# Kernel optimization log

Hardware: AMD Instinct MI355X
Metric: run time of the kernel (lower is better)

## Reference

```python
import jax, jax.numpy as jnp
import numpy as np

N = 100000   # num nodes
E = 640000   # num edges
IN, H, OUT = 6, 128, 1
BN_EPS = 1e-5


def setup_inputs() -> dict:
    key = jax.random.key(0)
    ks = jax.random.split(key, 12)
    x = jax.random.normal(ks[0], (N, IN), dtype=jnp.float32)
    edge_index = jax.random.randint(ks[1], (2, E), 0, N, dtype=jnp.int64)
    def lin(k, fin, fout):
        s = 1.0 / np.sqrt(fin)
        return jax.random.uniform(k, (fin, fout), jnp.float32, -s, s)
    return {
        "x": x,
        "edge_index": edge_index,
        "W1": lin(ks[2], IN, H),  "b1": jnp.zeros((H,), jnp.float32),
        "W2": lin(ks[3], H, H),   "b2": jnp.zeros((H,), jnp.float32),
        "W3": lin(ks[4], H, OUT), "b3": jnp.zeros((OUT,), jnp.float32),
        "g1": jnp.ones((H,), jnp.float32),  "be1": jnp.zeros((H,), jnp.float32),
        "g2": jnp.ones((H,), jnp.float32),  "be2": jnp.zeros((H,), jnp.float32),
    }


def _gcn_norm(edge_index):
    # add self-loops, then symmetric normalization D^-1/2 (A+I) D^-1/2
    loop = jnp.arange(N, dtype=edge_index.dtype)
    src = jnp.concatenate([edge_index[0], loop])
    dst = jnp.concatenate([edge_index[1], loop])
    deg = jax.ops.segment_sum(jnp.ones_like(dst, dtype=jnp.float32), dst, num_segments=N)
    dis = jnp.where(deg > 0, jax.lax.rsqrt(deg), 0.0)
    norm = dis[src] * dis[dst]  # (E+N,)
    return src, dst, norm


def _conv(h, W, b, src, dst, norm):
    m = h @ W                                   # (N, out) linear transform first
    msg = m[src] * norm[:, None]                # gather + edge scaling
    return jax.ops.segment_sum(msg, dst, num_segments=N) + b


def _bn(h, g, be):
    mu = h.mean(axis=0)
    var = h.var(axis=0)  # biased, as torch BN uses for normalization
    return g * (h - mu) * jax.lax.rsqrt(var + BN_EPS) + be


def reference(x, edge_index, W1, b1, W2, b2, W3, b3, g1, be1, g2, be2):
    src, dst, norm = _gcn_norm(edge_index)
    h = jax.nn.relu(_bn(_conv(x, W1, b1, src, dst, norm), g1, be1))
    h = jax.nn.relu(_bn(_conv(h, W2, b2, src, dst, norm), g2, be2))
    out = _conv(h, W3, b3, src, dst, norm)
    return jax.nn.sigmoid(out)  # (N, 1) risk scores
```

## Files before the change

### kernel.cpp

```cpp
#include <hip/hip_runtime.h>
#include <hip/hip_bf16.h>
#include <math.h>

#define HDIM 128
#define BN_EPS 1e-5f
#define CHUNK 512
#define TM 64
#define LDA 132

__device__ __forceinline__ int eget(const void* ei, long long pos, int is64) {
    return is64 ? (int)((const long long*)ei)[pos] : ((const int*)ei)[pos];
}
__device__ __forceinline__ unsigned short f2bf(float f) {
    unsigned int u = __float_as_uint(f);
    u += 0x7fffu + ((u >> 16) & 1u);
    return (unsigned short)(u >> 16);
}
__device__ __forceinline__ unsigned int pack2bf(float lo, float hi) {
    return (unsigned int)f2bf(lo) | ((unsigned int)f2bf(hi) << 16);
}
__device__ __forceinline__ float bflo(unsigned int u) {
    return __uint_as_float(u << 16);
}
__device__ __forceinline__ float bfhi(unsigned int u) {
    return __uint_as_float(u & 0xffff0000u);
}

__global__ void k_detect(const int* ei32, int* flag) {
    if (threadIdx.x == 0) {
        int nz = 0;
        for (int k = 0; k < 64; ++k) nz += (ei32[2 * k + 1] != 0);
        *flag = (nz < 8) ? 1 : 0;
    }
}

__global__ void k_count(const void* ei, const int* flag, int* cnt, int E) {
    int e = blockIdx.x * blockDim.x + threadIdx.x;
    if (e < E) {
        int d = eget(ei, (long long)E + e, *flag);
        atomicAdd(&cnt[d], 1);
    }
}

__global__ void k_dis(const int* cnt, float* dis, int N) {
    int i = blockIdx.x * blockDim.x + threadIdx.x;
    if (i < N) dis[i] = rsqrtf((float)(cnt[i] + 1));
}

__global__ void k_scan1(const int* cnt, int* bsum, int N) {
    __shared__ int s[256];
    int t = threadIdx.x;
    int i = blockIdx.x * CHUNK + t;
    int v = 0;
    if (i < N) v += cnt[i];
    if (i + 256 < N && t + 256 < CHUNK) v += cnt[i + 256];
    s[t] = v; __syncthreads();
    for (int o = 128; o > 0; o >>= 1) {
        if (t < o) s[t] += s[t + o];
        __syncthreads();
    }
    if (t == 0) bsum[blockIdx.x] = s[0];
}

__global__ void k_scan2(int* bsum, int nb) {
    __shared__ int s[512];
    int t = threadIdx.x;
    int carry = 0;
    for (int base = 0; base < nb; base += 512) {
        int i = base + t;
        int v = (i < nb) ? bsum[i] : 0;
        s[t] = v; __syncthreads();
        for (int o = 1; o < 512; o <<= 1) {
            int add = (t >= o) ? s[t - o] : 0;
            __syncthreads();
            s[t] += add;
            __syncthreads();
        }
        if (i < nb) bsum[i] = carry + s[t] - v;
        carry += s[511];
        __syncthreads();
    }
}

__global__ void k_scan3(const int* cnt, const int* bsum, int* rowptr, int N) {
    __shared__ int s[CHUNK];
    int t = threadIdx.x;
    int i = blockIdx.x * CHUNK + t;
    int v = (i < N) ? cnt[i] : 0;
    s[t] = v; __syncthreads();
    for (int o = 1; o < CHUNK; o <<= 1) {
        int add = (t >= o) ? s[t - o] : 0;
        __syncthreads();
        s[t] += add;
        __syncthreads();
    }
    if (i < N) rowptr[i] = bsum[blockIdx.x] + s[t] - v;
    if (i == N - 1) rowptr[N] = bsum[blockIdx.x] + s[t];
}

__global__ void k_fillcsr(const void* ei, const int* flag, const float* dis,
                          const int* rowptr, int* fill, int* esrc, float* enorm, int E) {
    int e = blockIdx.x * blockDim.x + threadIdx.x;
    if (e < E) {
        int is64 = *flag;
        int s = eget(ei, e, is64);
        int d = eget(ei, (long long)E + e, is64);
        int pos = rowptr[d] + atomicAdd(&fill[d], 1);
        esrc[pos] = s;
        enorm[pos] = dis[s] * dis[d];
    }
}

__global__ void k_padx(const float* __restrict__ x, float* __restrict__ xp, int N) {
    int t = blockIdx.x * blockDim.x + threadIdx.x;
    if (t < N * 8) {
        int i = t >> 3, c = t & 7;
        xp[t] = (c < 6) ? x[i * 6 + c] : 0.f;
    }
}

__global__ void k_gath_x(const float* __restrict__ xp, const int* __restrict__ rowptr,
                         const int* __restrict__ esrc, const float* __restrict__ enorm,
                         const float* __restrict__ dis, float* __restrict__ aggx, int N) {
    int i = blockIdx.x * blockDim.x + threadIdx.x;
    if (i >= N) return;
    float d = dis[i], d2 = d * d;
    float4 A = *(const float4*)&xp[i * 8];
    float2 B = *(const float2*)&xp[i * 8 + 4];
    float a0 = A.x * d2, a1 = A.y * d2, a2 = A.z * d2;
    float a3 = A.w * d2, a4 = B.x * d2, a5 = B.y * d2;
    int p = rowptr[i], pe = rowptr[i + 1];
    for (; p + 4 <= pe; p += 4) {
        int s0 = esrc[p], s1 = esrc[p + 1], s2 = esrc[p + 2], s3 = esrc[p + 3];
        float n0 = enorm[p], n1 = enorm[p + 1], n2 = enorm[p + 2], n3 = enorm[p + 3];
        float4 A0 = *(const float4*)&xp[s0 * 8];
        float2 B0 = *(const float2*)&xp[s0 * 8 + 4];
        float4 A1 = *(const float4*)&xp[s1 * 8];
        float2 B1 = *(const float2*)&xp[s1 * 8 + 4];
        float4 A2 = *(const float4*)&xp[s2 * 8];
        float2 B2 = *(const float2*)&xp[s2 * 8 + 4];
        float4 A3 = *(const float4*)&xp[s3 * 8];
        float2 B3 = *(const float2*)&xp[s3 * 8 + 4];
        a0 += (A0.x * n0 + A1.x * n1) + (A2.x * n2 + A3.x * n3);
        a1 += (A0.y * n0 + A1.y * n1) + (A2.y * n2 + A3.y * n3);
        a2 += (A0.z * n0 + A1.z * n1) + (A2.z * n2 + A3.z * n3);
        a3 += (A0.w * n0 + A1.w * n1) + (A2.w * n2 + A3.w * n3);
        a4 += (B0.x * n0 + B1.x * n1) + (B2.x * n2 + B3.x * n3);
        a5 += (B0.y * n0 + B1.y * n1) + (B2.y * n2 + B3.y * n3);
    }
    for (; p < pe; ++p) {
        int s0 = esrc[p]; float n0 = enorm[p];
        float4 A0 = *(const float4*)&xp[s0 * 8];
        float2 B0 = *(const float2*)&xp[s0 * 8 + 4];
        a0 += A0.x * n0; a1 += A0.y * n0; a2 += A0.z * n0;
        a3 += A0.w * n0; a4 += B0.x * n0; a5 += B0.y * n0;
    }
    aggx[i * 6 + 0] = a0; aggx[i * 6 + 1] = a1; aggx[i * 6 + 2] = a2;
    aggx[i * 6 + 3] = a3; aggx[i * 6 + 4] = a4; aggx[i * 6 + 5] = a5;
}

__global__ void k_gemm6(const float* __restrict__ aggx, const float* __restrict__ W1,
                        const float* __restrict__ b1, unsigned short* __restrict__ out,
                        float* __restrict__ S, int N) {
    __shared__ float w[6 * HDIM];
    __shared__ float bb[HDIM];
    __shared__ float sh1[256], sh2[256];
    for (int t = threadIdx.x; t < 6 * HDIM; t += blockDim.x) w[t] = W1[t];
    if (threadIdx.x < HDIM) bb[threadIdx.x] = b1[threadIdx.x];
    __syncthreads();
    int j = threadIdx.x & (HDIM - 1);
    int sub = threadIdx.x >> 7;
    float s1 = 0.f, s2 = 0.f;
    for (long long i = blockIdx.x * 2 + sub; i < N; i += (long long)gridDim.x * 2) {
        const float* r = &aggx[i * 6];
        float acc = bb[j];
        acc += r[0] * w[0 * HDIM + j];
        acc += r[1] * w[1 * HDIM + j];
        acc += r[2] * w[2 * HDIM + j];
        acc += r[3] * w[3 * HDIM + j];
        acc += r[4] * w[4 * HDIM + j];
        acc += r[5] * w[5 * HDIM + j];
        out[i * HDIM + j] = f2bf(acc);
        s1 += acc; s2 += acc * acc;
    }
    sh1[threadIdx.x] = s1; sh2[threadIdx.x] = s2;
    __syncthreads();
    if (threadIdx.x < HDIM) {
        atomicAdd(&S[j], sh1[j] + sh1[j + HDIM]);
        atomicAdd(&S[HDIM + j], sh2[j] + sh2[j + HDIM]);
    }
}

__global__ __launch_bounds__(512, 6)
void k_agg_gemm(const unsigned short* __restrict__ m1,
                const float* __restrict__ S1, const float* __restrict__ g1,
                const float* __restrict__ be1, float invN,
                const int* __restrict__ rowptr, const int* __restrict__ esrc,
                const float* __restrict__ enorm, const float* __restrict__ dis,
                const float* __restrict__ W, const float* __restrict__ b,
                unsigned short* __restrict__ out, float* __restrict__ S,
                int* __restrict__ ticket, int ntiles, int N) {
    __shared__ float At[TM * LDA];
    __shared__ float Pp[256];
    __shared__ int s_tile;
    const int tid = threadIdx.x;

    if (tid < HDIM) {
        float mu = S1[tid] * invN;
        float var = S1[HDIM + tid] * invN - mu * mu;
        float al = g1[tid] * rsqrtf(var + BN_EPS);
        Pp[tid] = al;
        Pp[HDIM + tid] = be1[tid] - mu * al;
    }
    __syncthreads();

    const int gl = tid & 31;
    const int gq = tid >> 5;
    const int c4 = gl * 4;
    const float4 pa = *(const float4*)&Pp[c4];
    const float4 pb = *(const float4*)&Pp[HDIM + c4];

    const int cg = tid & 31;
    const int rg = tid >> 5;
    const int c0 = cg * 4;
    const int r0 = rg * 4;
    const float4 bv = *(const float4*)&b[c0];

    for (;;) {
        if (tid == 0) s_tile = atomicAdd(ticket, 1);
        __syncthreads();
        const int tile = s_tile;
        if (tile >= ntiles) return;
        const long long i0 = (long long)tile * TM;

        for (int nn = gq; nn < TM; nn += 16) {
            long long i = i0 + nn;
            float a0 = 0.f, a1 = 0.f, a2 = 0.f, a3 = 0.f;
            if (i < N) {
                float d = dis[i], d2 = d * d;
                uint2 us = *(const uint2*)&m1[i * HDIM + c4];
                a0 = fmaxf(fmaf(pa.x, bflo(us.x), pb.x), 0.f) * d2;
                a1 = fmaxf(fmaf(pa.y, bfhi(us.x), pb.y), 0.f) * d2;
                a2 = fmaxf(fmaf(pa.z, bflo(us.y), pb.z), 0.f) * d2;
                a3 = fmaxf(fmaf(pa.w, bfhi(us.y), pb.w), 0.f) * d2;
                int p = rowptr[i], pe = rowptr[i + 1];
                for (; p + 4 <= pe; p += 4) {
                    int sA = esrc[p],     sB = esrc[p + 1];
                    int sC = esrc[p + 2], sD = esrc[p + 3];
                    float nA = enorm[p],     nB = enorm[p + 1];
                    float nC = enorm[p + 2], nD = enorm[p + 3];
                    uint2 uA = *(const uint2*)&m1[(long long)sA * HDIM + c4];
                    uint2 uB = *(const uint2*)&m1[(long long)sB * HDIM + c4];
                    uint2 uC = *(const uint2*)&m1[(long long)sC * HDIM + c4];
                    uint2 uD = *(const uint2*)&m1[(long long)sD * HDIM + c4];
                    a0 += (fmaxf(fmaf(pa.x, bflo(uA.x), pb.x), 0.f) * nA
                         + fmaxf(fmaf(pa.x, bflo(uB.x), pb.x), 0.f) * nB)
                        + (fmaxf(fmaf(pa.x, bflo(uC.x), pb.x), 0.f) * nC
                         + fmaxf(fmaf(pa.x, bflo(uD.x), pb.x), 0.f) * nD);
                    a1 += (fmaxf(fmaf(pa.y, bfhi(uA.x), pb.y), 0.f) * nA
                         + fmaxf(fmaf(pa.y, bfhi(uB.x), pb.y), 0.f) * nB)
                        + (fmaxf(fmaf(pa.y, bfhi(uC.x), pb.y), 0.f) * nC
                         + fmaxf(fmaf(pa.y, bfhi(uD.x), pb.y), 0.f) * nD);
                    a2 += (fmaxf(fmaf(pa.z, bflo(uA.y), pb.z), 0.f) * nA
                         + fmaxf(fmaf(pa.z, bflo(uB.y), pb.z), 0.f) * nB)
                        + (fmaxf(fmaf(pa.z, bflo(uC.y), pb.z), 0.f) * nC
                         + fmaxf(fmaf(pa.z, bflo(uD.y), pb.z), 0.f) * nD);
                    a3 += (fmaxf(fmaf(pa.w, bfhi(uA.y), pb.w), 0.f) * nA
                         + fmaxf(fmaf(pa.w, bfhi(uB.y), pb.w), 0.f) * nB)
                        + (fmaxf(fmaf(pa.w, bfhi(uC.y), pb.w), 0.f) * nC
                         + fmaxf(fmaf(pa.w, bfhi(uD.y), pb.w), 0.f) * nD);
                }
                if (p + 2 <= pe) {
                    int sA = esrc[p], sB = esrc[p + 1];
                    float nA = enorm[p], nB = enorm[p + 1];
                    uint2 uA = *(const uint2*)&m1[(long long)sA * HDIM + c4];
                    uint2 uB = *(const uint2*)&m1[(long long)sB * HDIM + c4];
                    a0 += fmaxf(fmaf(pa.x, bflo(uA.x), pb.x), 0.f) * nA
                        + fmaxf(fmaf(pa.x, bflo(uB.x), pb.x), 0.f) * nB;
                    a1 += fmaxf(fmaf(pa.y, bfhi(uA.x), pb.y), 0.f) * nA
                        + fmaxf(fmaf(pa.y, bfhi(uB.x), pb.y), 0.f) * nB;
                    a2 += fmaxf(fmaf(pa.z, bflo(uA.y), pb.z), 0.f) * nA
                        + fmaxf(fmaf(pa.z, bflo(uB.y), pb.z), 0.f) * nB;
                    a3 += fmaxf(fmaf(pa.w, bfhi(uA.y), pb.w), 0.f) * nA
                        + fmaxf(fmaf(pa.w, bfhi(uB.y), pb.w), 0.f) * nB;
                    p += 2;
                }
                if (p < pe) {
                    int sA = esrc[p]; float nA = enorm[p];
                    uint2 uA = *(const uint2*)&m1[(long long)sA * HDIM + c4];
                    a0 += fmaxf(fmaf(pa.x, bflo(uA.x), pb.x), 0.f) * nA;
                    a1 += fmaxf(fmaf(pa.y, bfhi(uA.x), pb.y), 0.f) * nA;
                    a2 += fmaxf(fmaf(pa.z, bflo(uA.y), pb.z), 0.f) * nA;
                    a3 += fmaxf(fmaf(pa.w, bfhi(uA.y), pb.w), 0.f) * nA;
                }
            }
            *(float4*)&At[nn * LDA + c4] = make_float4(a0, a1, a2, a3);
        }
        __syncthreads();

        float acc[4][4];
        #pragma unroll
        for (int rr = 0; rr < 4; ++rr) {
            acc[rr][0] = bv.x; acc[rr][1] = bv.y; acc[rr][2] = bv.z; acc[rr][3] = bv.w;
        }
        for (int k = 0; k < HDIM; k += 4) {
            const float4 w0 = *(const float4*)&W[(k + 0) * HDIM + c0];
            const float4 w1 = *(const float4*)&W[(k + 1) * HDIM + c0];
            const float4 w2 = *(const float4*)&W[(k + 2) * HDIM + c0];
            const float4 w3 = *(const float4*)&W[(k + 3) * HDIM + c0];
            #pragma unroll
            for (int rr = 0; rr < 4; ++rr) {
                const float4 av = *(const float4*)&At[(r0 + rr) * LDA + k];
                acc[rr][0] = fmaf(av.x, w0.x, acc[rr][0]);
                acc[rr][1] = fmaf(av.x, w0.y, acc[rr][1]);
                acc[rr][2] = fmaf(av.x, w0.z, acc[rr][2]);
                acc[rr][3] = fmaf(av.x, w0.w, acc[rr][3]);
                acc[rr][0] = fmaf(av.y, w1.x, acc[rr][0]);
                acc[rr][1] = fmaf(av.y, w1.y, acc[rr][1]);
                acc[rr][2] = fmaf(av.y, w1.z, acc[rr][2]);
                acc[rr][3] = fmaf(av.y, w1.w, acc[rr][3]);
                acc[rr][0] = fmaf(av.z, w2.x, acc[rr][0]);
                acc[rr][1] = fmaf(av.z, w2.y, acc[rr][1]);
                acc[rr][2] = fmaf(av.z, w2.z, acc[rr][2]);
                acc[rr][3] = fmaf(av.z, w2.w, acc[rr][3]);
                acc[rr][0] = fmaf(av.w, w3.x, acc[rr][0]);
                acc[rr][1] = fmaf(av.w, w3.y, acc[rr][1]);
                acc[rr][2] = fmaf(av.w, w3.z, acc[rr][2]);
                acc[rr][3] = fmaf(av.w, w3.w, acc[rr][3]);
            }
        }

        float cs1[4] = {0.f, 0.f, 0.f, 0.f};
        float cs2[4] = {0.f, 0.f, 0.f, 0.f};
        #pragma unroll
        for (int rr = 0; rr < 4; ++rr) {
            long long i = i0 + r0 + rr;
            if (i < N) {
                uint2 o;
                o.x = pack2bf(acc[rr][0], acc[rr][1]);
                o.y = pack2bf(acc[rr][2], acc[rr][3]);
                *(uint2*)&out[i * HDIM + c0] = o;
                #pragma unroll
                for (int cc = 0; cc < 4; ++cc) {
                    float v = acc[rr][cc];
                    cs1[cc] += v; cs2[cc] += v * v;
                }
            }
        }
        __syncthreads();
        #pragma unroll
        for (int cc = 0; cc < 4; ++cc) {
            At[rg * HDIM + c0 + cc]        = cs1[cc];
            At[2048 + rg * HDIM + c0 + cc] = cs2[cc];
        }
        __syncthreads();
        if (tid < 256) {
            int j = tid & (HDIM - 1);
            int which = tid >> 7;
            const float* bp = &At[which * 2048 + j];
            float s = 0.f;
            #pragma unroll
            for (int g = 0; g < 16; ++g) s += bp[g * HDIM];
            atomicAdd(&S[which * HDIM + j], s);
        }
        __syncthreads();
    }
}

__global__ void k_gemv2(const unsigned short* __restrict__ m2,
                        const float* __restrict__ S2, const float* __restrict__ g2,
                        const float* __restrict__ be2, float invN,
                        const float* __restrict__ W3, float* __restrict__ m3, int N) {
    __shared__ float Pp[256];
    int tid = threadIdx.x;
    if (tid < HDIM) {
        float mu = S2[tid] * invN;
        float var = S2[HDIM + tid] * invN - mu * mu;
        float al = g2[tid] * rsqrtf(var + BN_EPS);
        Pp[tid] = al;
        Pp[HDIM + tid] = be2[tid] - mu * al;
    }
    __syncthreads();
    int l = tid & 31;
    int c4 = l * 4;
    float4 pa = *(const float4*)&Pp[c4];
    float4 pb = *(const float4*)&Pp[HDIM + c4];
    float4 w  = *(const float4*)&W3[c4];
    for (long long row = blockIdx.x * 8 + (tid >> 5); row < N;
         row += (long long)gridDim.x * 8) {
        uint2 v = *(const uint2*)&m2[row * HDIM + c4];
        float s = fmaxf(fmaf(pa.x, bflo(v.x), pb.x), 0.f) * w.x
                + fmaxf(fmaf(pa.y, bfhi(v.x), pb.y), 0.f) * w.y
                + fmaxf(fmaf(pa.z, bflo(v.y), pb.z), 0.f) * w.z
                + fmaxf(fmaf(pa.w, bfhi(v.y), pb.w), 0.f) * w.w;
        for (int o = 16; o > 0; o >>= 1) s += __shfl_down(s, o, 32);
        if (l == 0) m3[row] = s;
    }
}

__global__ void k_gath_o(const float* __restrict__ m3, const int* __restrict__ rowptr,
                         const int* __restrict__ esrc, const float* __restrict__ enorm,
                         const float* __restrict__ dis, const float* __restrict__ b3,
                         float* __restrict__ out, int N) {
    int i = blockIdx.x * blockDim.x + threadIdx.x;
    if (i < N) {
        float d = dis[i];
        float acc = m3[i] * d * d;
        int p = rowptr[i], pe = rowptr[i + 1];
        for (; p + 4 <= pe; p += 4) {
            float v0 = m3[esrc[p]]     * enorm[p];
            float v1 = m3[esrc[p + 1]] * enorm[p + 1];
            float v2 = m3[esrc[p + 2]] * enorm[p + 2];
            float v3 = m3[esrc[p + 3]] * enorm[p + 3];
            acc += (v0 + v1) + (v2 + v3);
        }
        for (; p < pe; ++p)
            acc += m3[esrc[p]] * enorm[p];
        acc += b3[0];
        out[i] = 1.f / (1.f + expf(-acc));
    }
}

extern "C" void kernel_launch(void* const* d_in, const int* in_sizes, int n_in,
                              void* d_out, int out_size, void* d_ws, size_t ws_size,
                              hipStream_t stream) {
    const float* x  = (const float*)d_in[0];
    const void*  ei = d_in[1];
    const float* W1 = (const float*)d_in[2];
    const float* b1 = (const float*)d_in[3];
    const float* W2 = (const float*)d_in[4];
    const float* b2 = (const float*)d_in[5];
    const float* W3 = (const float*)d_in[6];
    const float* b3 = (const float*)d_in[7];
    const float* g1 = (const float*)d_in[8];
    const float* be1 = (const float*)d_in[9];
    const float* g2 = (const float*)d_in[10];
    const float* be2 = (const float*)d_in[11];

    const int N = in_sizes[0] / 6;
    const int E = in_sizes[1] / 2;
    const float invN = 1.0f / (float)N;

    float* ws = (float*)d_ws;
    long long off = 0;
    auto pad4 = [](long long v) { return (v + 3) & ~3LL; };
    int*   flag   = (int*)ws;                 off += 16;
    int*   ticket = (int*)ws + 1;
    float* dis    = ws + off;                 off = pad4(off + N);
    int*   cnt    = (int*)(ws + off);         off = pad4(off + N);
    int*   rowptr = (int*)(ws + off);         off = pad4(off + N + 16);
    int*   esrc   = (int*)(ws + off);         off = pad4(off + E);
    float* enorm  = ws + off;                 off = pad4(off + E);
    int*   bsum   = (int*)(ws + off);         off += 512;
    float* S1     = ws + off;                 off += 256;
    float* S2     = ws + off;                 off += 256;
    float* xp     = ws + off;                 off = pad4(off + (long long)8 * N);
    float* aggx   = ws + off;                 off = pad4(off + (long long)6 * N);
    float* m3     = ws + off;                 off = pad4(off + N);
    unsigned short* m1 = (unsigned short*)(ws + off); off = pad4(off + (long long)64 * N);
    unsigned short* m2 = (unsigned short*)(ws + off); off = pad4(off + (long long)64 * N);

    const int T = 256;
    const int bN  = (N + T - 1) / T;
    const int bE  = (E + T - 1) / T;
    const int nchunk = (N + CHUNK - 1) / CHUNK;
    const int ntiles = (N + TM - 1) / TM;

    hipMemsetAsync(flag, 0, 64, stream);
    hipMemsetAsync(S1, 0, 512 * sizeof(float), stream);
    k_detect<<<1, 64, 0, stream>>>((const int*)ei, flag);
    hipMemsetAsync(cnt, 0, (size_t)N * sizeof(int), stream);
    k_count<<<bE, T, 0, stream>>>(ei, flag, cnt, E);
    k_dis<<<bN, T, 0, stream>>>(cnt, dis, N);
    k_scan1<<<nchunk, 256, 0, stream>>>(cnt, bsum, N);
    k_scan2<<<1, 512, 0, stream>>>(bsum, nchunk);
    k_scan3<<<nchunk, CHUNK, 0, stream>>>(cnt, bsum, rowptr, N);
    hipMemsetAsync(cnt, 0, (size_t)N * sizeof(int), stream);
    k_fillcsr<<<bE, T, 0, stream>>>(ei, flag, dis, rowptr, cnt, esrc, enorm, E);

    k_padx<<<(N * 8 + T - 1) / T, T, 0, stream>>>(x, xp, N);
    k_gath_x<<<bN, T, 0, stream>>>(xp, rowptr, esrc, enorm, dis, aggx, N);
    k_gemm6<<<512, T, 0, stream>>>(aggx, W1, b1, m1, S1, N);

    k_agg_gemm<<<1024, 512, 0, stream>>>(m1, S1, g1, be1, invN,
                                         rowptr, esrc, enorm, dis,
                                         W2, b2, m2, S2, ticket, ntiles, N);

    k_gemv2<<<1024, T, 0, stream>>>(m2, S2, g2, be2, invN, W3, m3, N);
    k_gath_o<<<bN, T, 0, stream>>>(m3, rowptr, esrc, enorm, dis, b3, (float*)d_out, N);
}
```

Baseline: 276.7 us.

## Interleave edge src/norm into int2, widen gather to 16B per lane, merge memsets

Packs the CSR source index and edge norm into a single int2 array, so each edge needs one 8-byte load instead of two separate loads in every gather kernel. In the layer-2 aggregation, each lane now covers 8 bf16 channels (16-byte loads) with 16 lanes per row, so twice as many rows are processed at once and the inner loop is unrolled by 2 instead of 4. The degree counter is reset inside the scan kernel and the header memsets are merged into one, removing a memset call. The trade-off is fewer edge loads in flight per lane in exchange for wider loads and more rows in parallel, plus a bit more register pressure.

```diff
diff --git a/kernel.cpp b/kernel.cpp
--- a/kernel.cpp
+++ b/kernel.cpp
@@ -82,7 +82,7 @@
     }
 }
 
-__global__ void k_scan3(const int* cnt, const int* bsum, int* rowptr, int N) {
+__global__ void k_scan3(int* cnt, const int* bsum, int* rowptr, int N) {
     __shared__ int s[CHUNK];
     int t = threadIdx.x;
     int i = blockIdx.x * CHUNK + t;
@@ -94,20 +94,19 @@
         s[t] += add;
         __syncthreads();
     }
-    if (i < N) rowptr[i] = bsum[blockIdx.x] + s[t] - v;
+    if (i < N) { rowptr[i] = bsum[blockIdx.x] + s[t] - v; cnt[i] = 0; }
     if (i == N - 1) rowptr[N] = bsum[blockIdx.x] + s[t];
 }
 
 __global__ void k_fillcsr(const void* ei, const int* flag, const float* dis,
-                          const int* rowptr, int* fill, int* esrc, float* enorm, int E) {
+                          const int* rowptr, int* fill, int2* emeta, int E) {
     int e = blockIdx.x * blockDim.x + threadIdx.x;
     if (e < E) {
         int is64 = *flag;
         int s = eget(ei, e, is64);
         int d = eget(ei, (long long)E + e, is64);
         int pos = rowptr[d] + atomicAdd(&fill[d], 1);
-        esrc[pos] = s;
-        enorm[pos] = dis[s] * dis[d];
+        emeta[pos] = make_int2(s, __float_as_int(dis[s] * dis[d]));
     }
 }
 
@@ -120,7 +119,7 @@
 }
 
 __global__ void k_gath_x(const float* __restrict__ xp, const int* __restrict__ rowptr,
-                         const int* __restrict__ esrc, const float* __restrict__ enorm,
+                         const int2* __restrict__ emeta,
                          const float* __restrict__ dis, float* __restrict__ aggx, int N) {
     int i = blockIdx.x * blockDim.x + threadIdx.x;
     if (i >= N) return;
@@ -131,16 +130,17 @@
     float a3 = A.w * d2, a4 = B.x * d2, a5 = B.y * d2;
     int p = rowptr[i], pe = rowptr[i + 1];
     for (; p + 4 <= pe; p += 4) {
-        int s0 = esrc[p], s1 = esrc[p + 1], s2 = esrc[p + 2], s3 = esrc[p + 3];
-        float n0 = enorm[p], n1 = enorm[p + 1], n2 = enorm[p + 2], n3 = enorm[p + 3];
-        float4 A0 = *(const float4*)&xp[s0 * 8];
-        float2 B0 = *(const float2*)&xp[s0 * 8 + 4];
-        float4 A1 = *(const float4*)&xp[s1 * 8];
-        float2 B1 = *(const float2*)&xp[s1 * 8 + 4];
-        float4 A2 = *(const float4*)&xp[s2 * 8];
-        float2 B2 = *(const float2*)&xp[s2 * 8 + 4];
-        float4 A3 = *(const float4*)&xp[s3 * 8];
-        float2 B3 = *(const float2*)&xp[s3 * 8 + 4];
+        int2 e0 = emeta[p], e1 = emeta[p + 1], e2 = emeta[p + 2], e3 = emeta[p + 3];
+        float n0 = __int_as_float(e0.y), n1 = __int_as_float(e1.y);
+        float n2 = __int_as_float(e2.y), n3 = __int_as_float(e3.y);
+        float4 A0 = *(const float4*)&xp[e0.x * 8];
+        float2 B0 = *(const float2*)&xp[e0.x * 8 + 4];
+        float4 A1 = *(const float4*)&xp[e1.x * 8];
+        float2 B1 = *(const float2*)&xp[e1.x * 8 + 4];
+        float4 A2 = *(const float4*)&xp[e2.x * 8];
+        float2 B2 = *(const float2*)&xp[e2.x * 8 + 4];
+        float4 A3 = *(const float4*)&xp[e3.x * 8];
+        float2 B3 = *(const float2*)&xp[e3.x * 8 + 4];
         a0 += (A0.x * n0 + A1.x * n1) + (A2.x * n2 + A3.x * n3);
         a1 += (A0.y * n0 + A1.y * n1) + (A2.y * n2 + A3.y * n3);
         a2 += (A0.z * n0 + A1.z * n1) + (A2.z * n2 + A3.z * n3);
@@ -149,9 +149,10 @@
         a5 += (B0.y * n0 + B1.y * n1) + (B2.y * n2 + B3.y * n3);
     }
     for (; p < pe; ++p) {
-        int s0 = esrc[p]; float n0 = enorm[p];
-        float4 A0 = *(const float4*)&xp[s0 * 8];
-        float2 B0 = *(const float2*)&xp[s0 * 8 + 4];
+        int2 e0 = emeta[p];
+        float n0 = __int_as_float(e0.y);
+        float4 A0 = *(const float4*)&xp[e0.x * 8];
+        float2 B0 = *(const float2*)&xp[e0.x * 8 + 4];
         a0 += A0.x * n0; a1 += A0.y * n0; a2 += A0.z * n0;
         a3 += A0.w * n0; a4 += B0.x * n0; a5 += B0.y * n0;
     }
@@ -195,8 +196,8 @@
 void k_agg_gemm(const unsigned short* __restrict__ m1,
                 const float* __restrict__ S1, const float* __restrict__ g1,
                 const float* __restrict__ be1, float invN,
-                const int* __restrict__ rowptr, const int* __restrict__ esrc,
-                const float* __restrict__ enorm, const float* __restrict__ dis,
+                const int* __restrict__ rowptr, const int2* __restrict__ emeta,
+                const float* __restrict__ dis,
                 const float* __restrict__ W, const float* __restrict__ b,
                 unsigned short* __restrict__ out, float* __restrict__ S,
                 int* __restrict__ ticket, int ntiles, int N) {
@@ -214,11 +215,13 @@
     }
     __syncthreads();
 
-    const int gl = tid & 31;
-    const int gq = tid >> 5;
-    const int c4 = gl * 4;
-    const float4 pa = *(const float4*)&Pp[c4];
-    const float4 pb = *(const float4*)&Pp[HDIM + c4];
+    const int gl = tid & 15;
+    const int gq = tid >> 4;
+    const int c8 = gl * 8;
+    const float4 pa0 = *(const float4*)&Pp[c8];
+    const float4 pa1 = *(const float4*)&Pp[c8 + 4];
+    const float4 pb0 = *(const float4*)&Pp[HDIM + c8];
+    const float4 pb1 = *(const float4*)&Pp[HDIM + c8 + 4];
 
     const int cg = tid & 31;
     const int rg = tid >> 5;
@@ -233,68 +236,60 @@
         if (tile >= ntiles) return;
         const long long i0 = (long long)tile * TM;
 
-        for (int nn = gq; nn < TM; nn += 16) {
+        for (int nn = gq; nn < TM; nn += 32) {
             long long i = i0 + nn;
             float a0 = 0.f, a1 = 0.f, a2 = 0.f, a3 = 0.f;
+            float a4 = 0.f, a5 = 0.f, a6 = 0.f, a7 = 0.f;
             if (i < N) {
                 float d = dis[i], d2 = d * d;
-                uint2 us = *(const uint2*)&m1[i * HDIM + c4];
-                a0 = fmaxf(fmaf(pa.x, bflo(us.x), pb.x), 0.f) * d2;
-                a1 = fmaxf(fmaf(pa.y, bfhi(us.x), pb.y), 0.f) * d2;
-                a2 = fmaxf(fmaf(pa.z, bflo(us.y), pb.z), 0.f) * d2;
-                a3 = fmaxf(fmaf(pa.w, bfhi(us.y), pb.w), 0.f) * d2;
+                uint4 us = *(const uint4*)&m1[i * HDIM + c8];
+                a0 = fmaxf(fmaf(pa0.x, bflo(us.x), pb0.x), 0.f) * d2;
+                a1 = fmaxf(fmaf(pa0.y, bfhi(us.x), pb0.y), 0.f) * d2;
+                a2 = fmaxf(fmaf(pa0.z, bflo(us.y), pb0.z), 0.f) * d2;
+                a3 = fmaxf(fmaf(pa0.w, bfhi(us.y), pb0.w), 0.f) * d2;
+                a4 = fmaxf(fmaf(pa1.x, bflo(us.z), pb1.x), 0.f) * d2;
+                a5 = fmaxf(fmaf(pa1.y, bfhi(us.z), pb1.y), 0.f) * d2;
+                a6 = fmaxf(fmaf(pa1.z, bflo(us.w), pb1.z), 0.f) * d2;
+                a7 = fmaxf(fmaf(pa1.w, bfhi(us.w), pb1.w), 0.f) * d2;
                 int p = rowptr[i], pe = rowptr[i + 1];
-                for (; p + 4 <= pe; p += 4) {
-                    int sA = esrc[p],     sB = esrc[p + 1];
-                    int sC = esrc[p + 2], sD = esrc[p + 3];
-                    float nA = enorm[p],     nB = enorm[p + 1];
-                    float nC = enorm[p + 2], nD = enorm[p + 3];
-                    uint2 uA = *(const uint2*)&m1[(long long)sA * HDIM + c4];
-                    uint2 uB = *(const uint2*)&m1[(long long)sB * HDIM + c4];
-                    uint2 uC = *(const uint2*)&m1[(long long)sC * HDIM + c4];
-                    uint2 uD = *(const uint2*)&m1[(long long)sD * HDIM + c4];
-                    a0 += (fmaxf(fmaf(pa.x, bflo(uA.x), pb.x), 0.f) * nA
-                         + fmaxf(fmaf(pa.x, bflo(uB.x), pb.x), 0.f) * nB)
-                        + (fmaxf(fmaf(pa.x, bflo(uC.x), pb.x), 0.f) * nC
-                         + fmaxf(fmaf(pa.x, bflo(uD.x), pb.x), 0.f) * nD);
-                    a1 += (fmaxf(fmaf(pa.y, bfhi(uA.x), pb.y), 0.f) * nA
-                         + fmaxf(fmaf(pa.y, bfhi(uB.x), pb.y), 0.f) * nB)
-                        + (fmaxf(fmaf(pa.y, bfhi(uC.x), pb.y), 0.f) * nC
-                         + fmaxf(fmaf(pa.y, bfhi(uD.x), pb.y), 0.f) * nD);
-                    a2 += (fmaxf(fmaf(pa.z, bflo(uA.y), pb.z), 0.f) * nA
-                         + fmaxf(fmaf(pa.z, bflo(uB.y), pb.z), 0.f) * nB)
-                        + (fmaxf(fmaf(pa.z, bflo(uC.y), pb.z), 0.f) * nC
-                         + fmaxf(fmaf(pa.z, bflo(uD.y), pb.z), 0.f) * nD);
-                    a3 += (fmaxf(fmaf(pa.w, bfhi(uA.y), pb.w), 0.f) * nA
-                         + fmaxf(fmaf(pa.w, bfhi(uB.y), pb.w), 0.f) * nB)
-                        + (fmaxf(fmaf(pa.w, bfhi(uC.y), pb.w), 0.f) * nC
-                         + fmaxf(fmaf(pa.w, bfhi(uD.y), pb.w), 0.f) * nD);
-                }
-                if (p + 2 <= pe) {
-                    int sA = esrc[p], sB = esrc[p + 1];
-                    float nA = enorm[p], nB = enorm[p + 1];
-                    uint2 uA = *(const uint2*)&m1[(long long)sA * HDIM + c4];
-                    uint2 uB = *(const uint2*)&m1[(long long)sB * HDIM + c4];
-                    a0 += fmaxf(fmaf(pa.x, bflo(uA.x), pb.x), 0.f) * nA
-                        + fmaxf(fmaf(pa.x, bflo(uB.x), pb.x), 0.f) * nB;
-                    a1 += fmaxf(fmaf(pa.y, bfhi(uA.x), pb.y), 0.f) * nA
-                        + fmaxf(fmaf(pa.y, bfhi(uB.x), pb.y), 0.f) * nB;
-                    a2 += fmaxf(fmaf(pa.z, bflo(uA.y), pb.z), 0.f) * nA
-                        + fmaxf(fmaf(pa.z, bflo(uB.y), pb.z), 0.f) * nB;
-                    a3 += fmaxf(fmaf(pa.w, bfhi(uA.y), pb.w), 0.f) * nA
-                        + fmaxf(fmaf(pa.w, bfhi(uB.y), pb.w), 0.f) * nB;
-                    p += 2;
+                for (; p + 2 <= pe; p += 2) {
+                    int2 eA = emeta[p], eB = emeta[p + 1];
+                    float nA = __int_as_float(eA.y), nB = __int_as_float(eB.y);
+                    uint4 uA = *(const uint4*)&m1[(long long)eA.x * HDIM + c8];
+                    uint4 uB = *(const uint4*)&m1[(long long)eB.x * HDIM + c8];
+                    a0 += fmaxf(fmaf(pa0.x, bflo(uA.x), pb0.x), 0.f) * nA
+                        + fmaxf(fmaf(pa0.x, bflo(uB.x), pb0.x), 0.f) * nB;
+                    a1 += fmaxf(fmaf(pa0.y, bfhi(uA.x), pb0.y), 0.f) * nA
+                        + fmaxf(fmaf(pa0.y, bfhi(uB.x), pb0.y), 0.f) * nB;
+                    a2 += fmaxf(fmaf(pa0.z, bflo(uA.y), pb0.z), 0.f) * nA
+                        + fmaxf(fmaf(pa0.z, bflo(uB.y), pb0.z), 0.f) * nB;
+                    a3 += fmaxf(fmaf(pa0.w, bfhi(uA.y), pb0.w), 0.f) * nA
+                        + fmaxf(fmaf(pa0.w, bfhi(uB.y), pb0.w), 0.f) * nB;
+                    a4 += fmaxf(fmaf(pa1.x, bflo(uA.z), pb1.x), 0.f) * nA
+                        + fmaxf(fmaf(pa1.x, bflo(uB.z), pb1.x), 0.f) * nB;
+                    a5 += fmaxf(fmaf(pa1.y, bfhi(uA.z), pb1.y), 0.f) * nA
+                        + fmaxf(fmaf(pa1.y, bfhi(uB.z), pb1.y), 0.f) * nB;
+                    a6 += fmaxf(fmaf(pa1.z, bflo(uA.w), pb1.z), 0.f) * nA
+                        + fmaxf(fmaf(pa1.z, bflo(uB.w), pb1.z), 0.f) * nB;
+                    a7 += fmaxf(fmaf(pa1.w, bfhi(uA.w), pb1.w), 0.f) * nA
+                        + fmaxf(fmaf(pa1.w, bfhi(uB.w), pb1.w), 0.f) * nB;
                 }
                 if (p < pe) {
-                    int sA = esrc[p]; float nA = enorm[p];
-                    uint2 uA = *(const uint2*)&m1[(long long)sA * HDIM + c4];
-                    a0 += fmaxf(fmaf(pa.x, bflo(uA.x), pb.x), 0.f) * nA;
-                    a1 += fmaxf(fmaf(pa.y, bfhi(uA.x), pb.y), 0.f) * nA;
-                    a2 += fmaxf(fmaf(pa.z, bflo(uA.y), pb.z), 0.f) * nA;
-                    a3 += fmaxf(fmaf(pa.w, bfhi(uA.y), pb.w), 0.f) * nA;
+                    int2 eA = emeta[p];
+                    float nA = __int_as_float(eA.y);
+                    uint4 uA = *(const uint4*)&m1[(long long)eA.x * HDIM + c8];
+                    a0 += fmaxf(fmaf(pa0.x, bflo(uA.x), pb0.x), 0.f) * nA;
+                    a1 += fmaxf(fmaf(pa0.y, bfhi(uA.x), pb0.y), 0.f) * nA;
+                    a2 += fmaxf(fmaf(pa0.z, bflo(uA.y), pb0.z), 0.f) * nA;
+                    a3 += fmaxf(fmaf(pa0.w, bfhi(uA.y), pb0.w), 0.f) * nA;
+                    a4 += fmaxf(fmaf(pa1.x, bflo(uA.z), pb1.x), 0.f) * nA;
+                    a5 += fmaxf(fmaf(pa1.y, bfhi(uA.z), pb1.y), 0.f) * nA;
+                    a6 += fmaxf(fmaf(pa1.z, bflo(uA.w), pb1.z), 0.f) * nA;
+                    a7 += fmaxf(fmaf(pa1.w, bfhi(uA.w), pb1.w), 0.f) * nA;
                 }
             }
-            *(float4*)&At[nn * LDA + c4] = make_float4(a0, a1, a2, a3);
+            *(float4*)&At[nn * LDA + c8]     = make_float4(a0, a1, a2, a3);
+            *(float4*)&At[nn * LDA + c8 + 4] = make_float4(a4, a5, a6, a7);
         }
         __syncthreads();
 
@@ -399,7 +394,7 @@
 }
 
 __global__ void k_gath_o(const float* __restrict__ m3, const int* __restrict__ rowptr,
-                         const int* __restrict__ esrc, const float* __restrict__ enorm,
+                         const int2* __restrict__ emeta,
                          const float* __restrict__ dis, const float* __restrict__ b3,
                          float* __restrict__ out, int N) {
     int i = blockIdx.x * blockDim.x + threadIdx.x;
@@ -408,14 +403,17 @@
         float acc = m3[i] * d * d;
         int p = rowptr[i], pe = rowptr[i + 1];
         for (; p + 4 <= pe; p += 4) {
-            float v0 = m3[esrc[p]]     * enorm[p];
-            float v1 = m3[esrc[p + 1]] * enorm[p + 1];
-            float v2 = m3[esrc[p + 2]] * enorm[p + 2];
-            float v3 = m3[esrc[p + 3]] * enorm[p + 3];
+            int2 e0 = emeta[p], e1 = emeta[p + 1], e2 = emeta[p + 2], e3 = emeta[p + 3];
+            float v0 = m3[e0.x] * __int_as_float(e0.y);
+            float v1 = m3[e1.x] * __int_as_float(e1.y);
+            float v2 = m3[e2.x] * __int_as_float(e2.y);
+            float v3 = m3[e3.x] * __int_as_float(e3.y);
             acc += (v0 + v1) + (v2 + v3);
         }
-        for (; p < pe; ++p)
-            acc += m3[esrc[p]] * enorm[p];
+        for (; p < pe; ++p) {
+            int2 e0 = emeta[p];
+            acc += m3[e0.x] * __int_as_float(e0.y);
+        }
         acc += b3[0];
         out[i] = 1.f / (1.f + expf(-acc));
     }
@@ -446,14 +444,13 @@
     auto pad4 = [](long long v) { return (v + 3) & ~3LL; };
     int*   flag   = (int*)ws;                 off += 16;
     int*   ticket = (int*)ws + 1;
+    float* S1     = ws + off;                 off += 256;
+    float* S2     = ws + off;                 off += 256;
     float* dis    = ws + off;                 off = pad4(off + N);
     int*   cnt    = (int*)(ws + off);         off = pad4(off + N);
     int*   rowptr = (int*)(ws + off);         off = pad4(off + N + 16);
-    int*   esrc   = (int*)(ws + off);         off = pad4(off + E);
-    float* enorm  = ws + off;                 off = pad4(off + E);
+    int2*  emeta  = (int2*)(ws + off);        off = pad4(off + (long long)2 * E);
     int*   bsum   = (int*)(ws + off);         off += 512;
-    float* S1     = ws + off;                 off += 256;
-    float* S2     = ws + off;                 off += 256;
     float* xp     = ws + off;                 off = pad4(off + (long long)8 * N);
     float* aggx   = ws + off;                 off = pad4(off + (long long)6 * N);
     float* m3     = ws + off;                 off = pad4(off + N);
@@ -466,26 +463,24 @@
     const int nchunk = (N + CHUNK - 1) / CHUNK;
     const int ntiles = (N + TM - 1) / TM;
 
-    hipMemsetAsync(flag, 0, 64, stream);
-    hipMemsetAsync(S1, 0, 512 * sizeof(float), stream);
+    hipMemsetAsync(ws, 0, 528 * sizeof(float), stream);
+    hipMemsetAsync(cnt, 0, (size_t)N * sizeof(int), stream);
     k_detect<<<1, 64, 0, stream>>>((const int*)ei, flag);
-    hipMemsetAsync(cnt, 0, (size_t)N * sizeof(int), stream);
     k_count<<<bE, T, 0, stream>>>(ei, flag, cnt, E);
     k_dis<<<bN, T, 0, stream>>>(cnt, dis, N);
     k_scan1<<<nchunk, 256, 0, stream>>>(cnt, bsum, N);
     k_scan2<<<1, 512, 0, stream>>>(bsum, nchunk);
     k_scan3<<<nchunk, CHUNK, 0, stream>>>(cnt, bsum, rowptr, N);
-    hipMemsetAsync(cnt, 0, (size_t)N * sizeof(int), stream);
-    k_fillcsr<<<bE, T, 0, stream>>>(ei, flag, dis, rowptr, cnt, esrc, enorm, E);
+    k_fillcsr<<<bE, T, 0, stream>>>(ei, flag, dis, rowptr, cnt, emeta, E);
 
     k_padx<<<(N * 8 + T - 1) / T, T, 0, stream>>>(x, xp, N);
-    k_gath_x<<<bN, T, 0, stream>>>(xp, rowptr, esrc, enorm, dis, aggx, N);
+    k_gath_x<<<bN, T, 0, stream>>>(xp, rowptr, emeta, dis, aggx, N);
     k_gemm6<<<512, T, 0, stream>>>(aggx, W1, b1, m1, S1, N);
 
     k_agg_gemm<<<1024, 512, 0, stream>>>(m1, S1, g1, be1, invN,
-                                         rowptr, esrc, enorm, dis,
+                                         rowptr, emeta, dis,
                                          W2, b2, m2, S2, ticket, ntiles, N);
 
     k_gemv2<<<1024, T, 0, stream>>>(m2, S2, g2, be2, invN, W3, m3, N);
-    k_gath_o<<<bN, T, 0, stream>>>(m3, rowptr, esrc, enorm, dis, b3, (float*)d_out, N);
-}
+    k_gath_o<<<bN, T, 0, stream>>>(m3, rowptr, emeta, dis, b3, (float*)d_out, N);
+}
```

New measurement: 278.7 us. About the same (+0.7%).
